# Kernel optimization log

Hardware: AMD Instinct MI355X
Metric: run time of the kernel (lower is better)

The kernel has to match this reference:

```python
import jax, jax.numpy as jnp
import numpy as np

N, E, IN, HID, OUT, B = 50000, 800000, 128, 128, 64, 4096
EPS = 1e-5


def setup_inputs() -> dict:
    key = jax.random.key(0)
    ks = jax.random.split(key, 12)
    x = jax.random.normal(ks[0], (N, IN), jnp.float32)
    edge_index = jax.random.randint(ks[1], (2, E), 0, N, dtype=jnp.int32).astype(jnp.int64)
    target_index = jax.random.randint(ks[2], (B,), 0, N, dtype=jnp.int32).astype(jnp.int64)

    def lin(k, i, o):
        return jax.random.normal(k, (i, o), jnp.float32) * (1.0 / np.sqrt(i))

    return {
        'x': x, 'edge_index': edge_index, 'target_index': target_index,
        'W0': lin(ks[3], IN, HID), 'b0': jnp.zeros((HID,), jnp.float32),
        'W1': lin(ks[4], HID, HID), 'b1': jnp.zeros((HID,), jnp.float32),
        'W2': lin(ks[5], HID, HID), 'b2': jnp.zeros((HID,), jnp.float32),
        'g0': jnp.ones((HID,), jnp.float32), 'bt0': jnp.zeros((HID,), jnp.float32),
        'g1': jnp.ones((HID,), jnp.float32), 'bt1': jnp.zeros((HID,), jnp.float32),
        'f1w': lin(ks[6], HID, HID), 'f1b': jnp.zeros((HID,), jnp.float32),
        'f2w': lin(ks[7], HID, OUT), 'f2b': jnp.zeros((OUT,), jnp.float32),
    }


def _gcn_layer(h, W, b, src, dst, norm):
    # GCNConv: D^-1/2 (A+I) D^-1/2 (h W) + b  (self-loops already in src/dst)
    h = h @ W                                        # [N, out]
    msg = h[src] * norm[:, None]                     # [E+N, out]
    return jax.ops.segment_sum(msg, dst, num_segments=N) + b


def _batchnorm(h, g, bt):
    mu = jnp.mean(h, axis=0)
    var = jnp.mean((h - mu) ** 2, axis=0)            # biased, as torch BN
    return g * (h - mu) * jax.lax.rsqrt(var + EPS) + bt


def reference(x, edge_index, target_index, W0, b0, W1, b1, W2, b2,
              g0, bt0, g1, bt1, f1w, f1b, f2w, f2b):
    loop = jnp.arange(N, dtype=edge_index.dtype)
    src = jnp.concatenate([edge_index[0], loop])
    dst = jnp.concatenate([edge_index[1], loop])
    deg = jax.ops.segment_sum(jnp.ones_like(dst, jnp.float32), dst, num_segments=N)
    dinv = jax.lax.rsqrt(deg)                        # deg >= 1 via self-loops
    norm = dinv[src] * dinv[dst]                     # [E+N]

    h = _gcn_layer(x, W0, b0, src, dst, norm)
    h = jax.nn.relu(_batchnorm(h, g0, bt0))
    h = _gcn_layer(h, W1, b1, src, dst, norm)
    h = jax.nn.relu(_batchnorm(h, g1, bt1))
    h = _gcn_layer(h, W2, b2, src, dst, norm)

    # target_index.unsqueeze(1).expand(-1,-1) -> [B,1]; pool squeezes dim 1
    t = h[target_index]                              # [B, HID]
    t = jax.nn.relu(t @ f1w + f1b)                   # FeedForwardNetwork layer1 (dropout=0)
    return t @ f2w + f2b                             # [B, OUT]
```

## Files before the change

### kernel.cpp

```cpp
#include <hip/hip_runtime.h>


static const int GNN5566_NN  = 50000;
static const int GNN5566_NE  = 800000;
static const int GNN5566_NB  = 4096;
static const int GNN5566_CAP = 64;

static const int GNN5566_NBUCK  = (GNN5566_NN + 63) / 64;
static const int GNN5566_NCHUNK = 128;
static const int GNN5566_CHUNK  = GNN5566_NE / GNN5566_NCHUNK;

static const int GNN5566_WSLOT = 17408;

typedef short gnn5566_s16x8 __attribute__((ext_vector_type(8)));
typedef float gnn5566_f32x4 __attribute__((ext_vector_type(4)));

static __device__ inline float gnn5566_b2f(unsigned short h){
  return __uint_as_float(((unsigned int)h) << 16);
}
static __device__ inline unsigned short gnn5566_f2b(float f){
  unsigned int u = __float_as_uint(f);
  u += 0x7fffu + ((u >> 16) & 1u);
  return (unsigned short)(u >> 16);
}
static __device__ inline float gnn5566_loadf(const void* p, long long i, int isF32){
  if (isF32) return ((const float*)p)[i];
  return gnn5566_b2f(((const unsigned short*)p)[i]);
}

__global__ void GNNEncoder_5566277616090_detect(const int* ei, const int* tgt,
                                                const void* W0, int* flags,
                                                float* stats){
  int t = threadIdx.x;
  if (t < 512) stats[t] = 0.0f;
  if (t < 64) {
    int o1 = ei[2*t + 1];
    int o2 = tgt[2*t + 1];
    unsigned int w = ((const unsigned int*)W0)[t];
    unsigned int e = (w >> 7) & 255u;
    int bf16ish = (e >= 96u && e <= 134u) ? 1 : 0;
    unsigned long long m1 = __ballot(o1 != 0);
    unsigned long long m2 = __ballot(o2 != 0);
    unsigned long long m3 = __ballot(bf16ish);
    if (t == 0) {
      flags[0] = (m1 == 0ull) ? 1 : 0;
      flags[1] = (m2 == 0ull) ? 1 : 0;
      flags[2] = (__popcll(m3) >= 56) ? 0 : 1;
    }
  }
}

__global__ void GNNEncoder_5566277616090_wprep(const void* W0, const void* W1,
                                               const void* W2, const void* f1w,
                                               const void* f2w, unsigned short* wT,
                                               const int* flags){
  __shared__ unsigned short lt[128][129];
  int b = blockIdx.x, tid = threadIdx.x;
  const void* src = (b == 0) ? W0 : (b == 1) ? W1 : (b == 2) ? W2
                  : (b == 3) ? f1w : f2w;
  int wide = (b != 4);
  int f32 = flags[2];
  int tot = wide ? 16384 : 8192;
  for (int i = tid; i < tot; i += 256) {
    int k = wide ? (i >> 7) : (i >> 6);
    int c = wide ? (i & 127) : (i & 63);
    lt[k][c] = f32 ? gnn5566_f2b(((const float*)src)[i])
                   : ((const unsigned short*)src)[i];
  }
  __syncthreads();
  unsigned short* out = wT + b * GNN5566_WSLOT;
  int wtot = wide ? 2048 : 1024;
  for (int j = tid; j < wtot; j += 256) {
    int c = j >> 4, k8 = (j & 15) << 3;
    unsigned int p0 = (unsigned int)lt[k8    ][c] | ((unsigned int)lt[k8 + 1][c] << 16);
    unsigned int p1 = (unsigned int)lt[k8 + 2][c] | ((unsigned int)lt[k8 + 3][c] << 16);
    unsigned int p2 = (unsigned int)lt[k8 + 4][c] | ((unsigned int)lt[k8 + 5][c] << 16);
    unsigned int p3 = (unsigned int)lt[k8 + 6][c] | ((unsigned int)lt[k8 + 7][c] << 16);
    uint4 v; v.x = p0; v.y = p1; v.z = p2; v.w = p3;
    *(uint4*)(out + c * 136 + k8) = v;
  }
}

__global__ void GNNEncoder_5566277616090_fillH(const int* ei, unsigned int* histT,
                                               const int* flags){
  __shared__ int h[GNN5566_NBUCK];
  int tid = threadIdx.x, chunk = blockIdx.x;
  for (int b = tid; b < GNN5566_NBUCK; b += 256) h[b] = 0;
  __syncthreads();
  int f = flags[0];
  int base = chunk * GNN5566_CHUNK;
  for (int i = tid; i < GNN5566_CHUNK; i += 256) {
    int e = base + i;
    int d = f ? ei[2*(GNN5566_NE + e)] : ei[GNN5566_NE + e];
    atomicAdd(&h[d >> 6], 1);
  }
  __syncthreads();
  for (int b = tid; b < GNN5566_NBUCK; b += 256)
    histT[b * GNN5566_NCHUNK + chunk] = (unsigned int)h[b];
}

__global__ void GNNEncoder_5566277616090_fillS1(unsigned int* histT, int* btot){
  int wv   = (int)(blockIdx.x * 4u + (threadIdx.x >> 6));
  int lane = threadIdx.x & 63;
  if (wv >= GNN5566_NBUCK) return;
  unsigned int* row = histT + wv * GNN5566_NCHUNK;
  uint2 v = ((const uint2*)row)[lane];
  int a = (int)v.x, b = (int)v.y;
  int s = a + b;
  int incl = s;
  #pragma unroll
  for (int off = 1; off < 64; off <<= 1) {
    int t = __shfl_up(incl, off, 64);
    if (lane >= off) incl += t;
  }
  int excl = incl - s;
  uint2 o; o.x = (unsigned int)excl; o.y = (unsigned int)(excl + a);
  ((uint2*)row)[lane] = o;
  if (lane == 63) btot[wv] = incl;
}

__global__ void GNNEncoder_5566277616090_fillS2(const int* btot, int* segStart){
  __shared__ int a[1024];
  int tid = threadIdx.x;
  int own = (tid < GNN5566_NBUCK) ? btot[tid] : 0;
  a[tid] = own;
  __syncthreads();
  for (int off = 1; off < 1024; off <<= 1) {
    int v = (tid >= off) ? a[tid - off] : 0;
    __syncthreads();
    a[tid] += v;
    __syncthreads();
  }
  if (tid < GNN5566_NBUCK) segStart[tid] = a[tid] - own;
  if (tid == 0) segStart[GNN5566_NBUCK] = GNN5566_NE;
}

__global__ void GNNEncoder_5566277616090_fillScatter(const int* ei,
                                                     const unsigned int* histT,
                                                     const int* segStart,
                                                     unsigned int* sorted,
                                                     const int* flags){
  __shared__ int cur[GNN5566_NBUCK];
  int tid = threadIdx.x, chunk = blockIdx.x;
  for (int b = tid; b < GNN5566_NBUCK; b += 256)
    cur[b] = (int)histT[b * GNN5566_NCHUNK + chunk] + segStart[b];
  __syncthreads();
  int f = flags[0];
  int base = chunk * GNN5566_CHUNK;
  for (int i = tid; i < GNN5566_CHUNK; i += 256) {
    int e = base + i;
    int s = f ? ei[2*e]                : ei[e];
    int d = f ? ei[2*(GNN5566_NE + e)] : ei[GNN5566_NE + e];
    int p = atomicAdd(&cur[d >> 6], 1);
    sorted[p] = ((unsigned int)s << 6) | (unsigned int)(d & 63);
  }
}

__global__ void GNNEncoder_5566277616090_fillB(const int* segStart,
                                               const unsigned int* sorted,
                                               unsigned short* colIdx16, int* cnt,
                                               float* dinv){
  __shared__ unsigned int lbuf[64 * 32];
  __shared__ int lcnt[64];
  int b   = blockIdx.x;
  int tid = threadIdx.x;
  if (tid < 64) lcnt[tid] = 0;
  __syncthreads();

  int s0 = segStart[b];
  int n  = segStart[b + 1] - s0;
  const unsigned int* bp = sorted + s0;
  unsigned short* lists = (unsigned short*)lbuf;
  for (int i = tid; i < n; i += 256) {
    unsigned int w = bp[i];
    int d = (int)(w & 63u);
    int s = (int)(w >> 6);
    int p = atomicAdd(&lcnt[d], 1);
    if (p < GNN5566_CAP) lists[d * 64 + p] = (unsigned short)s;
  }
  __syncthreads();

  if (tid < 64) {
    int node = b * 64 + tid;
    if (node < GNN5566_NN) {
      int c = lcnt[tid];
      cnt[node]  = c;
      dinv[node] = rsqrtf((float)(c + 1));
    }
  }
  unsigned int* out = (unsigned int*)colIdx16;
  for (int idx = tid; idx < 2048; idx += 256) {
    int d = idx >> 5;
    int node = b * 64 + d;
    if (node < GNN5566_NN)
      out[(long long)node * 32 + (idx & 31)] = lbuf[idx];
  }
}

__global__ void GNNEncoder_5566277616090_kernel(const void* A,
                                                const unsigned short* wT,
                                                unsigned short* Out, int nRows,
                                                const float* bnA, const float* bnC,
                                                const float* rowScale,
                                                const int* gather, const int* gatherFlag,
                                                const void* bias, int reluOut,
                                                int aExternal, const int* flags)
{
  __shared__ __align__(16) unsigned short gnnLw[128 * 136];
  int tid = threadIdx.x;
  int wF32 = flags[2];
  int aF32 = aExternal ? wF32 : 0;

  {
    const uint4* src = (const uint4*)wT;
    uint4* dst = (uint4*)gnnLw;
    for (int i = tid; i < 2176; i += 256) dst[i] = src[i];
  }
  __syncthreads();

  int wave = tid >> 6, lane = tid & 63;
  int q = lane >> 4, ln = lane & 15;
  int rowBase = blockIdx.x * 64 + wave * 16;
  int r  = rowBase + ln;
  int cr = (r < nRows) ? r : (nRows - 1);
  int ar = cr;
  if (gather) ar = (*gatherFlag) ? gather[2 * cr] : gather[cr];
  float rs = rowScale ? rowScale[cr] : 1.0f;

  gnn5566_s16x8 afr[4];
  #pragma unroll
  for (int kk = 0; kk < 4; ++kk) {
    int kb = kk * 32 + q * 8;
    float vals[8];
    if (aF32) {
      const float4* ap = (const float4*)A + (long long)ar * 32 + (kb >> 2);
      float4 u = ap[0], w = ap[1];
      vals[0] = u.x; vals[1] = u.y; vals[2] = u.z; vals[3] = u.w;
      vals[4] = w.x; vals[5] = w.y; vals[6] = w.z; vals[7] = w.w;
    } else {
      const uint4* ap = (const uint4*)A + (long long)ar * 16 + (kb >> 3);
      uint4 u = ap[0];
      vals[0] = gnn5566_b2f((unsigned short)(u.x & 0xffffu));
      vals[1] = gnn5566_b2f((unsigned short)(u.x >> 16));
      vals[2] = gnn5566_b2f((unsigned short)(u.y & 0xffffu));
      vals[3] = gnn5566_b2f((unsigned short)(u.y >> 16));
      vals[4] = gnn5566_b2f((unsigned short)(u.z & 0xffffu));
      vals[5] = gnn5566_b2f((unsigned short)(u.z >> 16));
      vals[6] = gnn5566_b2f((unsigned short)(u.w & 0xffffu));
      vals[7] = gnn5566_b2f((unsigned short)(u.w >> 16));
    }
    #pragma unroll
    for (int j = 0; j < 8; ++j) {
      float v = vals[j];
      if (bnA) { int k = kb + j; v = fmaxf(v * bnA[k] + bnC[k], 0.0f); }
      afr[kk][j] = (short)gnn5566_f2b(v * rs);
    }
  }

  gnn5566_f32x4 zero4;
  zero4[0] = 0.0f; zero4[1] = 0.0f; zero4[2] = 0.0f; zero4[3] = 0.0f;
  gnn5566_f32x4 acc[8];
  #pragma unroll
  for (int t = 0; t < 8; ++t) acc[t] = zero4;

  #pragma unroll
  for (int kk = 0; kk < 4; ++kk) {
    int kb = kk * 32 + q * 8;
    #pragma unroll
    for (int t = 0; t < 8; ++t) {
      gnn5566_s16x8 bfr = *(const gnn5566_s16x8*)(&gnnLw[(t * 16 + ln) * 136 + kb]);
      acc[t] = __builtin_amdgcn_mfma_f32_16x16x32_bf16(afr[kk], bfr, acc[t], 0, 0, 0);
    }
  }

  #pragma unroll
  for (int t = 0; t < 8; ++t) {
    int col = t * 16 + ln;
    float badd = bias ? gnn5566_loadf(bias, col, wF32) : 0.0f;
    #pragma unroll
    for (int rg = 0; rg < 4; ++rg) {
      int grow = rowBase + q * 4 + rg;
      if (grow < nRows) {
        float v = acc[t][rg] + badd;
        if (reluOut) v = fmaxf(v, 0.0f);
        Out[(long long)grow * 128 + col] = gnn5566_f2b(v);
      }
    }
  }
}

__global__ void GNNEncoder_5566277616090_g64(const unsigned short* A,
                                             const unsigned short* wT,
                                             void* Out, int nRows,
                                             const void* bias, const int* flags)
{
  __shared__ __align__(16) unsigned short gnnLw[64 * 136];
  int tid = threadIdx.x;
  int f32 = flags[2];

  {
    const uint4* src = (const uint4*)wT;
    uint4* dst = (uint4*)gnnLw;
    for (int i = tid; i < 1088; i += 256) dst[i] = src[i];
  }
  __syncthreads();

  int wave = tid >> 6, lane = tid & 63;
  int q = lane >> 4, ln = lane & 15;
  int rowBase = blockIdx.x * 64 + wave * 16;
  int r  = rowBase + ln;
  int cr = (r < nRows) ? r : (nRows - 1);

  gnn5566_s16x8 afr[4];
  #pragma unroll
  for (int kk = 0; kk < 4; ++kk) {
    int kb = kk * 32 + q * 8;
    const uint4* ap = (const uint4*)A + (long long)cr * 16 + (kb >> 3);
    uint4 u = ap[0];
    unsigned short e[8];
    e[0] = (unsigned short)(u.x & 0xffffu); e[1] = (unsigned short)(u.x >> 16);
    e[2] = (unsigned short)(u.y & 0xffffu); e[3] = (unsigned short)(u.y >> 16);
    e[4] = (unsigned short)(u.z & 0xffffu); e[5] = (unsigned short)(u.z >> 16);
    e[6] = (unsigned short)(u.w & 0xffffu); e[7] = (unsigned short)(u.w >> 16);
    #pragma unroll
    for (int j = 0; j < 8; ++j) afr[kk][j] = (short)e[j];
  }

  gnn5566_f32x4 zero4;
  zero4[0] = 0.0f; zero4[1] = 0.0f; zero4[2] = 0.0f; zero4[3] = 0.0f;
  gnn5566_f32x4 acc[4];
  #pragma unroll
  for (int t = 0; t < 4; ++t) acc[t] = zero4;

  #pragma unroll
  for (int kk = 0; kk < 4; ++kk) {
    int kb = kk * 32 + q * 8;
    #pragma unroll
    for (int t = 0; t < 4; ++t) {
      gnn5566_s16x8 bfr = *(const gnn5566_s16x8*)(&gnnLw[(t * 16 + ln) * 136 + kb]);
      acc[t] = __builtin_amdgcn_mfma_f32_16x16x32_bf16(afr[kk], bfr, acc[t], 0, 0, 0);
    }
  }

  #pragma unroll
  for (int t = 0; t < 4; ++t) {
    int col = t * 16 + ln;
    float badd = gnn5566_loadf(bias, col, f32);
    #pragma unroll
    for (int rg = 0; rg < 4; ++rg) {
      int grow = rowBase + q * 4 + rg;
      if (grow < nRows) {
        float v = acc[t][rg] + badd;
        if (f32) ((float*)Out)[(long long)grow * 64 + col] = v;
        else     ((unsigned short*)Out)[(long long)grow * 64 + col] = gnn5566_f2b(v);
      }
    }
  }
}

__global__ void GNNEncoder_5566277616090_agg(const unsigned short* hs,
                                             const unsigned short* colIdx16,
                                             const int* cnt, const float* dinv,
                                             const void* bias, unsigned short* ha,
                                             const int* flags)
{
  int gw = (int)((blockIdx.x * 256u + threadIdx.x) >> 6);
  if (gw >= GNN5566_NN) return;
  int lane = threadIdx.x & 63;
  const unsigned int* hrow = (const unsigned int*)hs;
  unsigned int sv = hrow[(long long)gw * 64 + lane];
  float a0 = __uint_as_float(sv << 16);
  float a1 = __uint_as_float(sv & 0xffff0000u);
  int m = cnt[gw]; if (m > GNN5566_CAP) m = GNN5566_CAP;
  const unsigned short* cp = colIdx16 + (long long)gw * GNN5566_CAP;
  const uint4* cp4 = (const uint4*)cp;
  int i = 0;
  for (; i + 8 <= m; i += 8) {
    uint4 iw = cp4[i >> 3];
    unsigned int s0 = iw.x & 0xffffu, s1 = iw.x >> 16;
    unsigned int s2 = iw.y & 0xffffu, s3 = iw.y >> 16;
    unsigned int s4 = iw.z & 0xffffu, s5 = iw.z >> 16;
    unsigned int s6 = iw.w & 0xffffu, s7 = iw.w >> 16;
    unsigned int v0 = hrow[(long long)s0 * 64 + lane];
    unsigned int v1 = hrow[(long long)s1 * 64 + lane];
    unsigned int v2 = hrow[(long long)s2 * 64 + lane];
    unsigned int v3 = hrow[(long long)s3 * 64 + lane];
    unsigned int v4 = hrow[(long long)s4 * 64 + lane];
    unsigned int v5 = hrow[(long long)s5 * 64 + lane];
    unsigned int v6 = hrow[(long long)s6 * 64 + lane];
    unsigned int v7 = hrow[(long long)s7 * 64 + lane];
    a0 += __uint_as_float(v0 << 16) + __uint_as_float(v1 << 16)
        + __uint_as_float(v2 << 16) + __uint_as_float(v3 << 16)
        + __uint_as_float(v4 << 16) + __uint_as_float(v5 << 16)
        + __uint_as_float(v6 << 16) + __uint_as_float(v7 << 16);
    a1 += __uint_as_float(v0 & 0xffff0000u) + __uint_as_float(v1 & 0xffff0000u)
        + __uint_as_float(v2 & 0xffff0000u) + __uint_as_float(v3 & 0xffff0000u)
        + __uint_as_float(v4 & 0xffff0000u) + __uint_as_float(v5 & 0xffff0000u)
        + __uint_as_float(v6 & 0xffff0000u) + __uint_as_float(v7 & 0xffff0000u);
  }
  for (; i < m; ++i) {
    unsigned int v = hrow[(long long)cp[i] * 64 + lane];
    a0 += __uint_as_float(v << 16);
    a1 += __uint_as_float(v & 0xffff0000u);
  }
  float s = dinv[gw];
  int f32 = flags[2];
  float o0 = a0 * s + gnn5566_loadf(bias, lane * 2,     f32);
  float o1 = a1 * s + gnn5566_loadf(bias, lane * 2 + 1, f32);
  unsigned int packed = (unsigned int)gnn5566_f2b(o0)
                      | (((unsigned int)gnn5566_f2b(o1)) << 16);
  ((unsigned int*)ha)[(long long)gw * 64 + lane] = packed;
}

__global__ void GNNEncoder_5566277616090_stats(const unsigned short* ha, float* stats){
  __shared__ float red[256];
  const unsigned int* h32 = (const unsigned int*)ha;
  int tid = threadIdx.x;
  int cp2 = tid & 63, sub = tid >> 6;
  float s0 = 0.0f, s1 = 0.0f, q0 = 0.0f, q1 = 0.0f;
  for (int r = blockIdx.x * 4 + sub; r < GNN5566_NN; r += 1024) {
    unsigned int v = h32[(long long)r * 64 + cp2];
    float a = __uint_as_float(v << 16);
    float b = __uint_as_float(v & 0xffff0000u);
    s0 += a; q0 += a * a; s1 += b; q1 += b * b;
  }
  red[tid] = s0; __syncthreads();
  if (sub == 0) atomicAdd(&stats[2*cp2],
      red[cp2] + red[64+cp2] + red[128+cp2] + red[192+cp2]);
  __syncthreads();
  red[tid] = s1; __syncthreads();
  if (sub == 0) atomicAdd(&stats[2*cp2 + 1],
      red[cp2] + red[64+cp2] + red[128+cp2] + red[192+cp2]);
  __syncthreads();
  red[tid] = q0; __syncthreads();
  if (sub == 0) atomicAdd(&stats[128 + 2*cp2],
      red[cp2] + red[64+cp2] + red[128+cp2] + red[192+cp2]);
  __syncthreads();
  red[tid] = q1; __syncthreads();
  if (sub == 0) atomicAdd(&stats[128 + 2*cp2 + 1],
      red[cp2] + red[64+cp2] + red[128+cp2] + red[192+cp2]);
}

__global__ void GNNEncoder_5566277616090_bnfin(const float* stats, const void* g,
                                               const void* bt, float* bnA, float* bnC,
                                               const int* flags){
  int c = threadIdx.x;
  if (c >= 128) return;
  int f32 = flags[2];
  float invN = 1.0f / (float)GNN5566_NN;
  float mu  = stats[c] * invN;
  float var = stats[128 + c] * invN - mu * mu;
  if (var < 0.0f) var = 0.0f;
  float a = gnn5566_loadf(g, c, f32) * rsqrtf(var + 1e-5f);
  bnA[c] = a;
  bnC[c] = gnn5566_loadf(bt, c, f32) - mu * a;
}

extern "C" void kernel_launch(void* const* d_in, const int* in_sizes, int n_in,
                              void* d_out, int out_size, void* d_ws, size_t ws_size,
                              hipStream_t stream)
{
  const void* x   = d_in[0];
  const int*  ei  = (const int*)d_in[1];
  const int*  tgt = (const int*)d_in[2];
  const void* W0  = d_in[3];
  const void* b0  = d_in[4];
  const void* W1  = d_in[5];
  const void* b1  = d_in[6];
  const void* W2  = d_in[7];
  const void* b2  = d_in[8];
  const void* g0  = d_in[9];
  const void* bt0 = d_in[10];
  const void* g1  = d_in[11];
  const void* bt1 = d_in[12];
  const void* f1w = d_in[13];
  const void* f1b = d_in[14];
  const void* f2w = d_in[15];
  const void* fb2 = d_in[16];

  char* ws = (char*)d_ws;
  int*            segStart = (int*)           (ws + 0);
  int*            btot     = (int*)           (ws + 4096);
  int*            cnt      = (int*)           (ws + 8192);
  float*          dinv     = (float*)         (ws + 208896);
  unsigned short* wT       = (unsigned short*)(ws + 409600);
  unsigned int*   histT    = (unsigned int*)  (ws + 586752);
  unsigned int*   sorted   = (unsigned int*)  (ws + 987648);
  unsigned short* colIdx16 = (unsigned short*)(ws + 4188160);
  unsigned short* hs       = (unsigned short*)(ws + 10588160);
  unsigned short* ha       = (unsigned short*)(ws + 23388160);
  unsigned short* ub       = (unsigned short*)(ws + 36188160);
  float*          stats    = (float*)         (ws + 37236992);
  float*          bn       = (float*)         (ws + 37239040);
  int*            flags    = (int*)           (ws + 37241088);

  float* bn0A = bn;       float* bn0C = bn + 128;
  float* bn1A = bn + 256; float* bn1C = bn + 384;

  GNNEncoder_5566277616090_detect<<<1, 512, 0, stream>>>(ei, tgt, W0, flags, stats);
  GNNEncoder_5566277616090_wprep <<<5, 256, 0, stream>>>(W0, W1, W2, f1w, f2w, wT, flags);
  GNNEncoder_5566277616090_fillH <<<GNN5566_NCHUNK, 256, 0, stream>>>(ei, histT, flags);
  GNNEncoder_5566277616090_fillS1<<<196, 256, 0, stream>>>(histT, btot);
  GNNEncoder_5566277616090_fillS2<<<1, 1024, 0, stream>>>(btot, segStart);
  GNNEncoder_5566277616090_fillScatter<<<GNN5566_NCHUNK, 256, 0, stream>>>(
      ei, histT, segStart, sorted, flags);
  GNNEncoder_5566277616090_fillB <<<GNN5566_NBUCK, 256, 0, stream>>>(
      segStart, sorted, colIdx16, cnt, dinv);

  const int gemmGrid = (GNN5566_NN + 63) / 64;

  GNNEncoder_5566277616090_kernel<<<gemmGrid, 256, 0, stream>>>(
      x, wT, hs, GNN5566_NN, (const float*)0, (const float*)0, dinv,
      (const int*)0, (const int*)0, (const void*)0, 0, 1, flags);
  GNNEncoder_5566277616090_agg  <<<12500, 256, 0, stream>>>(hs, colIdx16, cnt, dinv, b0, ha, flags);
  GNNEncoder_5566277616090_stats<<<256, 256, 0, stream>>>(ha, stats);
  GNNEncoder_5566277616090_bnfin<<<1, 128, 0, stream>>>(stats, g0, bt0, bn0A, bn0C, flags);

  GNNEncoder_5566277616090_kernel<<<gemmGrid, 256, 0, stream>>>(
      ha, wT + GNN5566_WSLOT, hs, GNN5566_NN, bn0A, bn0C, dinv,
      (const int*)0, (const int*)0, (const void*)0, 0, 0, flags);
  GNNEncoder_5566277616090_agg  <<<12500, 256, 0, stream>>>(hs, colIdx16, cnt, dinv, b1, ha, flags);
  GNNEncoder_5566277616090_stats<<<256, 256, 0, stream>>>(ha, stats + 256);
  GNNEncoder_5566277616090_bnfin<<<1, 128, 0, stream>>>(stats + 256, g1, bt1, bn1A, bn1C, flags);

  GNNEncoder_5566277616090_kernel<<<gemmGrid, 256, 0, stream>>>(
      ha, wT + 2 * GNN5566_WSLOT, hs, GNN5566_NN, bn1A, bn1C, dinv,
      (const int*)0, (const int*)0, (const void*)0, 0, 0, flags);
  GNNEncoder_5566277616090_agg  <<<12500, 256, 0, stream>>>(hs, colIdx16, cnt, dinv, b2, ha, flags);

  GNNEncoder_5566277616090_kernel<<<64, 256, 0, stream>>>(
      ha, wT + 3 * GNN5566_WSLOT, ub, GNN5566_NB,
      (const float*)0, (const float*)0, (const float*)0,
      tgt, flags + 1, f1b, 1, 0, flags);
  GNNEncoder_5566277616090_g64<<<64, 256, 0, stream>>>(
      ub, wT + 4 * GNN5566_WSLOT, d_out, GNN5566_NB, fb2, flags);
}
```

Measured before the change: 387.1 us.

## Fuse small kernels, stage GEMM epilogue through LDS, fuse FFN layers

Several small launches are merged: flag detection moves into the weight-prep kernel, BN finalisation runs in the last block of the stats kernel via an atomic done counter, and the two FFN GEMMs become one kernel with the hidden tile kept in LDS. The main GEMM caches BN scale/shift and bias in shared memory and writes its output tile through LDS for coalesced 16-byte stores. The histogram chunk count doubles and the int64 index reads use int2 loads. The aim is to cut launch overhead and uncoalesced stores, at the cost of more LDS use and a last-block synchronisation pattern.

```diff
diff --git a/kernel.cpp b/kernel.cpp
--- a/kernel.cpp
+++ b/kernel.cpp
@@ -7,7 +7,7 @@
 static const int GNN5566_CAP = 64;
 
 static const int GNN5566_NBUCK  = (GNN5566_NN + 63) / 64;
-static const int GNN5566_NCHUNK = 128;
+static const int GNN5566_NCHUNK = 256;
 static const int GNN5566_CHUNK  = GNN5566_NE / GNN5566_NCHUNK;
 
 static const int GNN5566_WSLOT = 17408;
@@ -28,38 +28,47 @@
   return gnn5566_b2f(((const unsigned short*)p)[i]);
 }
 
-__global__ void GNNEncoder_5566277616090_detect(const int* ei, const int* tgt,
-                                                const void* W0, int* flags,
-                                                float* stats){
-  int t = threadIdx.x;
-  if (t < 512) stats[t] = 0.0f;
-  if (t < 64) {
-    int o1 = ei[2*t + 1];
-    int o2 = tgt[2*t + 1];
-    unsigned int w = ((const unsigned int*)W0)[t];
-    unsigned int e = (w >> 7) & 255u;
-    int bf16ish = (e >= 96u && e <= 134u) ? 1 : 0;
-    unsigned long long m1 = __ballot(o1 != 0);
-    unsigned long long m2 = __ballot(o2 != 0);
-    unsigned long long m3 = __ballot(bf16ish);
-    if (t == 0) {
-      flags[0] = (m1 == 0ull) ? 1 : 0;
-      flags[1] = (m2 == 0ull) ? 1 : 0;
-      flags[2] = (__popcll(m3) >= 56) ? 0 : 1;
-    }
-  }
-}
-
 __global__ void GNNEncoder_5566277616090_wprep(const void* W0, const void* W1,
                                                const void* W2, const void* f1w,
                                                const void* f2w, unsigned short* wT,
-                                               const int* flags){
+                                               const int* ei, const int* tgt,
+                                               int* flags, float* stats, int* done){
   __shared__ unsigned short lt[128][129];
+  __shared__ int sF32;
   int b = blockIdx.x, tid = threadIdx.x;
+
+  if (b == 5) {
+    for (int i = tid; i < 512; i += 256) stats[i] = 0.0f;
+    if (tid < 2) done[tid] = 0;
+    if (tid < 64) {
+      int o1 = ei[2*tid + 1];
+      int o2 = tgt[2*tid + 1];
+      unsigned int w = ((const unsigned int*)W0)[tid];
+      unsigned int e = (w >> 7) & 255u;
+      unsigned long long m1 = __ballot(o1 != 0);
+      unsigned long long m2 = __ballot(o2 != 0);
+      unsigned long long m3 = __ballot(e >= 96u && e <= 134u);
+      if (tid == 0) {
+        flags[0] = (m1 == 0ull) ? 1 : 0;
+        flags[1] = (m2 == 0ull) ? 1 : 0;
+        flags[2] = (__popcll(m3) >= 56) ? 0 : 1;
+      }
+    }
+    return;
+  }
+
+  if (tid < 64) {
+    unsigned int w = ((const unsigned int*)W0)[tid];
+    unsigned int e = (w >> 7) & 255u;
+    unsigned long long m3 = __ballot(e >= 96u && e <= 134u);
+    if (tid == 0) sF32 = (__popcll(m3) >= 56) ? 0 : 1;
+  }
+  __syncthreads();
+  int f32 = sF32;
+
   const void* src = (b == 0) ? W0 : (b == 1) ? W1 : (b == 2) ? W2
                   : (b == 3) ? f1w : f2w;
   int wide = (b != 4);
-  int f32 = flags[2];
   int tot = wide ? 16384 : 8192;
   for (int i = tid; i < tot; i += 256) {
     int k = wide ? (i >> 7) : (i >> 6);
@@ -91,7 +100,7 @@
   int base = chunk * GNN5566_CHUNK;
   for (int i = tid; i < GNN5566_CHUNK; i += 256) {
     int e = base + i;
-    int d = f ? ei[2*(GNN5566_NE + e)] : ei[GNN5566_NE + e];
+    int d = f ? ((const int2*)ei)[GNN5566_NE + e].x : ei[GNN5566_NE + e];
     atomicAdd(&h[d >> 6], 1);
   }
   __syncthreads();
@@ -104,9 +113,9 @@
   int lane = threadIdx.x & 63;
   if (wv >= GNN5566_NBUCK) return;
   unsigned int* row = histT + wv * GNN5566_NCHUNK;
-  uint2 v = ((const uint2*)row)[lane];
-  int a = (int)v.x, b = (int)v.y;
-  int s = a + b;
+  uint4 v = ((const uint4*)row)[lane];
+  int a = (int)v.x, b = (int)v.y, c = (int)v.z, d = (int)v.w;
+  int s = a + b + c + d;
   int incl = s;
   #pragma unroll
   for (int off = 1; off < 64; off <<= 1) {
@@ -114,8 +123,12 @@
     if (lane >= off) incl += t;
   }
   int excl = incl - s;
-  uint2 o; o.x = (unsigned int)excl; o.y = (unsigned int)(excl + a);
-  ((uint2*)row)[lane] = o;
+  uint4 o;
+  o.x = (unsigned int)excl;
+  o.y = (unsigned int)(excl + a);
+  o.z = (unsigned int)(excl + a + b);
+  o.w = (unsigned int)(excl + a + b + c);
+  ((uint4*)row)[lane] = o;
   if (lane == 63) btot[wv] = incl;
 }
 
@@ -149,8 +162,8 @@
   int base = chunk * GNN5566_CHUNK;
   for (int i = tid; i < GNN5566_CHUNK; i += 256) {
     int e = base + i;
-    int s = f ? ei[2*e]                : ei[e];
-    int d = f ? ei[2*(GNN5566_NE + e)] : ei[GNN5566_NE + e];
+    int s = f ? ((const int2*)ei)[e].x                : ei[e];
+    int d = f ? ((const int2*)ei)[GNN5566_NE + e].x   : ei[GNN5566_NE + e];
     int p = atomicAdd(&cur[d >> 6], 1);
     sorted[p] = ((unsigned int)s << 6) | (unsigned int)(d & 63);
   }
@@ -202,11 +215,11 @@
                                                 unsigned short* Out, int nRows,
                                                 const float* bnA, const float* bnC,
                                                 const float* rowScale,
-                                                const int* gather, const int* gatherFlag,
                                                 const void* bias, int reluOut,
                                                 int aExternal, const int* flags)
 {
   __shared__ __align__(16) unsigned short gnnLw[128 * 136];
+  __shared__ float lbnA[128], lbnC[128], lbias[128];
   int tid = threadIdx.x;
   int wF32 = flags[2];
   int aF32 = aExternal ? wF32 : 0;
@@ -215,6 +228,11 @@
     const uint4* src = (const uint4*)wT;
     uint4* dst = (uint4*)gnnLw;
     for (int i = tid; i < 2176; i += 256) dst[i] = src[i];
+  }
+  if (tid < 128) {
+    lbnA[tid]  = bnA  ? bnA[tid] : 0.0f;
+    lbnC[tid]  = bnC  ? bnC[tid] : 0.0f;
+    lbias[tid] = bias ? gnn5566_loadf(bias, tid, wF32) : 0.0f;
   }
   __syncthreads();
 
@@ -223,9 +241,8 @@
   int rowBase = blockIdx.x * 64 + wave * 16;
   int r  = rowBase + ln;
   int cr = (r < nRows) ? r : (nRows - 1);
-  int ar = cr;
-  if (gather) ar = (*gatherFlag) ? gather[2 * cr] : gather[cr];
   float rs = rowScale ? rowScale[cr] : 1.0f;
+  int useBN = (bnA != 0);
 
   gnn5566_s16x8 afr[4];
   #pragma unroll
@@ -233,12 +250,12 @@
     int kb = kk * 32 + q * 8;
     float vals[8];
     if (aF32) {
-      const float4* ap = (const float4*)A + (long long)ar * 32 + (kb >> 2);
+      const float4* ap = (const float4*)A + (long long)cr * 32 + (kb >> 2);
       float4 u = ap[0], w = ap[1];
       vals[0] = u.x; vals[1] = u.y; vals[2] = u.z; vals[3] = u.w;
       vals[4] = w.x; vals[5] = w.y; vals[6] = w.z; vals[7] = w.w;
     } else {
-      const uint4* ap = (const uint4*)A + (long long)ar * 16 + (kb >> 3);
+      const uint4* ap = (const uint4*)A + (long long)cr * 16 + (kb >> 3);
       uint4 u = ap[0];
       vals[0] = gnn5566_b2f((unsigned short)(u.x & 0xffffu));
       vals[1] = gnn5566_b2f((unsigned short)(u.x >> 16));
@@ -249,12 +266,20 @@
       vals[6] = gnn5566_b2f((unsigned short)(u.w & 0xffffu));
       vals[7] = gnn5566_b2f((unsigned short)(u.w >> 16));
     }
-    #pragma unroll
-    for (int j = 0; j < 8; ++j) {
-      float v = vals[j];
-      if (bnA) { int k = kb + j; v = fmaxf(v * bnA[k] + bnC[k], 0.0f); }
-      afr[kk][j] = (short)gnn5566_f2b(v * rs);
-    }
+    if (useBN) {
+      float4 a0 = *(const float4*)&lbnA[kb], a1 = *(const float4*)&lbnA[kb + 4];
+      float4 c0 = *(const float4*)&lbnC[kb], c1 = *(const float4*)&lbnC[kb + 4];
+      vals[0] = fmaxf(vals[0] * a0.x + c0.x, 0.0f);
+      vals[1] = fmaxf(vals[1] * a0.y + c0.y, 0.0f);
+      vals[2] = fmaxf(vals[2] * a0.z + c0.z, 0.0f);
+      vals[3] = fmaxf(vals[3] * a0.w + c0.w, 0.0f);
+      vals[4] = fmaxf(vals[4] * a1.x + c1.x, 0.0f);
+      vals[5] = fmaxf(vals[5] * a1.y + c1.y, 0.0f);
+      vals[6] = fmaxf(vals[6] * a1.z + c1.z, 0.0f);
+      vals[7] = fmaxf(vals[7] * a1.w + c1.w, 0.0f);
+    }
+    #pragma unroll
+    for (int j = 0; j < 8; ++j) afr[kk][j] = (short)gnn5566_f2b(vals[j] * rs);
   }
 
   gnn5566_f32x4 zero4;
@@ -273,49 +298,70 @@
     }
   }
 
+  __syncthreads();
   #pragma unroll
   for (int t = 0; t < 8; ++t) {
     int col = t * 16 + ln;
-    float badd = bias ? gnn5566_loadf(bias, col, wF32) : 0.0f;
+    float badd = lbias[col];
     #pragma unroll
     for (int rg = 0; rg < 4; ++rg) {
-      int grow = rowBase + q * 4 + rg;
-      if (grow < nRows) {
-        float v = acc[t][rg] + badd;
-        if (reluOut) v = fmaxf(v, 0.0f);
-        Out[(long long)grow * 128 + col] = gnn5566_f2b(v);
-      }
-    }
-  }
-}
-
-__global__ void GNNEncoder_5566277616090_g64(const unsigned short* A,
-                                             const unsigned short* wT,
-                                             void* Out, int nRows,
-                                             const void* bias, const int* flags)
+      float v = acc[t][rg] + badd;
+      if (reluOut) v = fmaxf(v, 0.0f);
+      gnnLw[(wave * 16 + q * 4 + rg) * 136 + col] = gnn5566_f2b(v);
+    }
+  }
+  __syncthreads();
+  int tRowBase = blockIdx.x * 64;
+  for (int j = tid; j < 1024; j += 256) {
+    int rr = j >> 4, c4 = j & 15;
+    int grow = tRowBase + rr;
+    if (grow < nRows) {
+      uint4 v = *(const uint4*)&gnnLw[rr * 136 + c4 * 8];
+      *(uint4*)&Out[(long long)grow * 128 + c4 * 8] = v;
+    }
+  }
+}
+
+__global__ void GNNEncoder_5566277616090_ffn(const unsigned short* A,
+                                             const unsigned short* wT3,
+                                             const unsigned short* wT4,
+                                             void* Out, const int* tgt,
+                                             const int* tgtFlag,
+                                             const void* f1b, const void* fb2,
+                                             const int* flags)
 {
-  __shared__ __align__(16) unsigned short gnnLw[64 * 136];
+  __shared__ __align__(16) unsigned short lwA[128 * 136];
+  __shared__ __align__(16) unsigned short lwB[64 * 136];
+  __shared__ __align__(16) unsigned short ep[64 * 136];
+  __shared__ float lb1[128];
+  __shared__ float lb2[64];
   int tid = threadIdx.x;
   int f32 = flags[2];
 
   {
-    const uint4* src = (const uint4*)wT;
-    uint4* dst = (uint4*)gnnLw;
-    for (int i = tid; i < 1088; i += 256) dst[i] = src[i];
-  }
+    const uint4* sA = (const uint4*)wT3;
+    uint4* dA = (uint4*)lwA;
+    for (int i = tid; i < 2176; i += 256) dA[i] = sA[i];
+    const uint4* sB = (const uint4*)wT4;
+    uint4* dB = (uint4*)lwB;
+    for (int i = tid; i < 1088; i += 256) dB[i] = sB[i];
+  }
+  if (tid < 128) lb1[tid] = gnn5566_loadf(f1b, tid, f32);
+  if (tid < 64)  lb2[tid] = gnn5566_loadf(fb2, tid, f32);
   __syncthreads();
 
   int wave = tid >> 6, lane = tid & 63;
   int q = lane >> 4, ln = lane & 15;
   int rowBase = blockIdx.x * 64 + wave * 16;
   int r  = rowBase + ln;
-  int cr = (r < nRows) ? r : (nRows - 1);
+  int cr = (r < GNN5566_NB) ? r : (GNN5566_NB - 1);
+  int ar = (*tgtFlag) ? tgt[2 * cr] : tgt[cr];
 
   gnn5566_s16x8 afr[4];
   #pragma unroll
   for (int kk = 0; kk < 4; ++kk) {
     int kb = kk * 32 + q * 8;
-    const uint4* ap = (const uint4*)A + (long long)cr * 16 + (kb >> 3);
+    const uint4* ap = (const uint4*)A + (long long)ar * 16 + (kb >> 3);
     uint4 u = ap[0];
     unsigned short e[8];
     e[0] = (unsigned short)(u.x & 0xffffu); e[1] = (unsigned short)(u.x >> 16);
@@ -328,29 +374,57 @@
 
   gnn5566_f32x4 zero4;
   zero4[0] = 0.0f; zero4[1] = 0.0f; zero4[2] = 0.0f; zero4[3] = 0.0f;
-  gnn5566_f32x4 acc[4];
-  #pragma unroll
-  for (int t = 0; t < 4; ++t) acc[t] = zero4;
-
+  gnn5566_f32x4 acc[8];
+  #pragma unroll
+  for (int t = 0; t < 8; ++t) acc[t] = zero4;
   #pragma unroll
   for (int kk = 0; kk < 4; ++kk) {
     int kb = kk * 32 + q * 8;
     #pragma unroll
+    for (int t = 0; t < 8; ++t) {
+      gnn5566_s16x8 bfr = *(const gnn5566_s16x8*)(&lwA[(t * 16 + ln) * 136 + kb]);
+      acc[t] = __builtin_amdgcn_mfma_f32_16x16x32_bf16(afr[kk], bfr, acc[t], 0, 0, 0);
+    }
+  }
+  #pragma unroll
+  for (int t = 0; t < 8; ++t) {
+    int col = t * 16 + ln;
+    float badd = lb1[col];
+    #pragma unroll
+    for (int rg = 0; rg < 4; ++rg) {
+      float v = fmaxf(acc[t][rg] + badd, 0.0f);
+      ep[(wave * 16 + q * 4 + rg) * 136 + col] = gnn5566_f2b(v);
+    }
+  }
+  __syncthreads();
+
+  gnn5566_s16x8 afr2[4];
+  #pragma unroll
+  for (int kk = 0; kk < 4; ++kk) {
+    int kb = kk * 32 + q * 8;
+    afr2[kk] = *(const gnn5566_s16x8*)(&ep[(wave * 16 + ln) * 136 + kb]);
+  }
+  gnn5566_f32x4 acc2[4];
+  #pragma unroll
+  for (int t = 0; t < 4; ++t) acc2[t] = zero4;
+  #pragma unroll
+  for (int kk = 0; kk < 4; ++kk) {
+    int kb = kk * 32 + q * 8;
+    #pragma unroll
     for (int t = 0; t < 4; ++t) {
-      gnn5566_s16x8 bfr = *(const gnn5566_s16x8*)(&gnnLw[(t * 16 + ln) * 136 + kb]);
-      acc[t] = __builtin_amdgcn_mfma_f32_16x16x32_bf16(afr[kk], bfr, acc[t], 0, 0, 0);
-    }
-  }
-
+      gnn5566_s16x8 bfr = *(const gnn5566_s16x8*)(&lwB[(t * 16 + ln) * 136 + kb]);
+      acc2[t] = __builtin_amdgcn_mfma_f32_16x16x32_bf16(afr2[kk], bfr, acc2[t], 0, 0, 0);
+    }
+  }
   #pragma unroll
   for (int t = 0; t < 4; ++t) {
     int col = t * 16 + ln;
-    float badd = gnn5566_loadf(bias, col, f32);
+    float badd = lb2[col];
     #pragma unroll
     for (int rg = 0; rg < 4; ++rg) {
       int grow = rowBase + q * 4 + rg;
-      if (grow < nRows) {
-        float v = acc[t][rg] + badd;
+      if (grow < GNN5566_NB) {
+        float v = acc2[t][rg] + badd;
         if (f32) ((float*)Out)[(long long)grow * 64 + col] = v;
         else     ((unsigned short*)Out)[(long long)grow * 64 + col] = gnn5566_f2b(v);
       }
@@ -412,8 +486,12 @@
   ((unsigned int*)ha)[(long long)gw * 64 + lane] = packed;
 }
 
-__global__ void GNNEncoder_5566277616090_stats(const unsigned short* ha, float* stats){
+__global__ void GNNEncoder_5566277616090_stats(const unsigned short* ha, float* statsL,
+                                               const void* g, const void* bt,
+                                               float* bnA, float* bnC,
+                                               const int* flags, int* doneCtr){
   __shared__ float red[256];
+  __shared__ int lastFlag;
   const unsigned int* h32 = (const unsigned int*)ha;
   int tid = threadIdx.x;
   int cp2 = tid & 63, sub = tid >> 6;
@@ -425,35 +503,37 @@
     s0 += a; q0 += a * a; s1 += b; q1 += b * b;
   }
   red[tid] = s0; __syncthreads();
-  if (sub == 0) atomicAdd(&stats[2*cp2],
+  if (sub == 0) atomicAdd(&statsL[2*cp2],
       red[cp2] + red[64+cp2] + red[128+cp2] + red[192+cp2]);
   __syncthreads();
   red[tid] = s1; __syncthreads();
-  if (sub == 0) atomicAdd(&stats[2*cp2 + 1],
+  if (sub == 0) atomicAdd(&statsL[2*cp2 + 1],
       red[cp2] + red[64+cp2] + red[128+cp2] + red[192+cp2]);
   __syncthreads();
   red[tid] = q0; __syncthreads();
-  if (sub == 0) atomicAdd(&stats[128 + 2*cp2],
+  if (sub == 0) atomicAdd(&statsL[128 + 2*cp2],
       red[cp2] + red[64+cp2] + red[128+cp2] + red[192+cp2]);
   __syncthreads();
   red[tid] = q1; __syncthreads();
-  if (sub == 0) atomicAdd(&stats[128 + 2*cp2 + 1],
+  if (sub == 0) atomicAdd(&statsL[128 + 2*cp2 + 1],
       red[cp2] + red[64+cp2] + red[128+cp2] + red[192+cp2]);
-}
-
-__global__ void GNNEncoder_5566277616090_bnfin(const float* stats, const void* g,
-                                               const void* bt, float* bnA, float* bnC,
-                                               const int* flags){
-  int c = threadIdx.x;
-  if (c >= 128) return;
-  int f32 = flags[2];
-  float invN = 1.0f / (float)GNN5566_NN;
-  float mu  = stats[c] * invN;
-  float var = stats[128 + c] * invN - mu * mu;
-  if (var < 0.0f) var = 0.0f;
-  float a = gnn5566_loadf(g, c, f32) * rsqrtf(var + 1e-5f);
-  bnA[c] = a;
-  bnC[c] = gnn5566_loadf(bt, c, f32) - mu * a;
+  __syncthreads();
+
+  __threadfence();
+  if (tid == 0) lastFlag = (atomicAdd(doneCtr, 1) == (int)gridDim.x - 1);
+  __syncthreads();
+  if (lastFlag && tid < 128) {
+    int f32 = flags[2];
+    float sum = atomicAdd(&statsL[tid], 0.0f);
+    float sq  = atomicAdd(&statsL[128 + tid], 0.0f);
+    float invN = 1.0f / (float)GNN5566_NN;
+    float mu  = sum * invN;
+    float var = sq * invN - mu * mu;
+    if (var < 0.0f) var = 0.0f;
+    float a = gnn5566_loadf(g, tid, f32) * rsqrtf(var + 1e-5f);
+    bnA[tid] = a;
+    bnC[tid] = gnn5566_loadf(bt, tid, f32) - mu * a;
+  }
 }
 
 extern "C" void kernel_launch(void* const* d_in, const int* in_sizes, int n_in,
@@ -484,21 +564,21 @@
   int*            cnt      = (int*)           (ws + 8192);
   float*          dinv     = (float*)         (ws + 208896);
   unsigned short* wT       = (unsigned short*)(ws + 409600);
-  unsigned int*   histT    = (unsigned int*)  (ws + 586752);
-  unsigned int*   sorted   = (unsigned int*)  (ws + 987648);
-  unsigned short* colIdx16 = (unsigned short*)(ws + 4188160);
-  unsigned short* hs       = (unsigned short*)(ws + 10588160);
-  unsigned short* ha       = (unsigned short*)(ws + 23388160);
-  unsigned short* ub       = (unsigned short*)(ws + 36188160);
-  float*          stats    = (float*)         (ws + 37236992);
-  float*          bn       = (float*)         (ws + 37239040);
-  int*            flags    = (int*)           (ws + 37241088);
+  unsigned int*   histT    = (unsigned int*)  (ws + 583936);
+  unsigned int*   sorted   = (unsigned int*)  (ws + 1384960);
+  unsigned short* colIdx16 = (unsigned short*)(ws + 4585216);
+  unsigned short* hs       = (unsigned short*)(ws + 10985472);
+  unsigned short* ha       = (unsigned short*)(ws + 23785728);
+  float*          stats    = (float*)         (ws + 36585984);
+  float*          bn       = (float*)         (ws + 36588032);
+  int*            flags    = (int*)           (ws + 36590080);
+  int*            done     = (int*)           (ws + 36590336);
 
   float* bn0A = bn;       float* bn0C = bn + 128;
   float* bn1A = bn + 256; float* bn1C = bn + 384;
 
-  GNNEncoder_5566277616090_detect<<<1, 512, 0, stream>>>(ei, tgt, W0, flags, stats);
-  GNNEncoder_5566277616090_wprep <<<5, 256, 0, stream>>>(W0, W1, W2, f1w, f2w, wT, flags);
+  GNNEncoder_5566277616090_wprep <<<6, 256, 0, stream>>>(
+      W0, W1, W2, f1w, f2w, wT, ei, tgt, flags, stats, done);
   GNNEncoder_5566277616090_fillH <<<GNN5566_NCHUNK, 256, 0, stream>>>(ei, histT, flags);
   GNNEncoder_5566277616090_fillS1<<<196, 256, 0, stream>>>(histT, btot);
   GNNEncoder_5566277616090_fillS2<<<1, 1024, 0, stream>>>(btot, segStart);
@@ -511,27 +591,24 @@
 
   GNNEncoder_5566277616090_kernel<<<gemmGrid, 256, 0, stream>>>(
       x, wT, hs, GNN5566_NN, (const float*)0, (const float*)0, dinv,
-      (const int*)0, (const int*)0, (const void*)0, 0, 1, flags);
+      (const void*)0, 0, 1, flags);
   GNNEncoder_5566277616090_agg  <<<12500, 256, 0, stream>>>(hs, colIdx16, cnt, dinv, b0, ha, flags);
-  GNNEncoder_5566277616090_stats<<<256, 256, 0, stream>>>(ha, stats);
-  GNNEncoder_5566277616090_bnfin<<<1, 128, 0, stream>>>(stats, g0, bt0, bn0A, bn0C, flags);
+  GNNEncoder_5566277616090_stats<<<256, 256, 0, stream>>>(
+      ha, stats, g0, bt0, bn0A, bn0C, flags, done);
 
   GNNEncoder_5566277616090_kernel<<<gemmGrid, 256, 0, stream>>>(
       ha, wT + GNN5566_WSLOT, hs, GNN5566_NN, bn0A, bn0C, dinv,
-      (const int*)0, (const int*)0, (const void*)0, 0, 0, flags);
+      (const void*)0, 0, 0, flags);
   GNNEncoder_5566277616090_agg  <<<12500, 256, 0, stream>>>(hs, colIdx16, cnt, dinv, b1, ha, flags);
-  GNNEncoder_5566277616090_stats<<<256, 256, 0, stream>>>(ha, stats + 256);
-  GNNEncoder_5566277616090_bnfin<<<1, 128, 0, stream>>>(stats + 256, g1, bt1, bn1A, bn1C, flags);
+  GNNEncoder_5566277616090_stats<<<256, 256, 0, stream>>>(
+      ha, stats + 256, g1, bt1, bn1A, bn1C, flags, done + 1);
 
   GNNEncoder_5566277616090_kernel<<<gemmGrid, 256, 0, stream>>>(
       ha, wT + 2 * GNN5566_WSLOT, hs, GNN5566_NN, bn1A, bn1C, dinv,
-      (const int*)0, (const int*)0, (const void*)0, 0, 0, flags);
+      (const void*)0, 0, 0, flags);
   GNNEncoder_5566277616090_agg  <<<12500, 256, 0, stream>>>(hs, colIdx16, cnt, dinv, b2, ha, flags);
 
-  GNNEncoder_5566277616090_kernel<<<64, 256, 0, stream>>>(
-      ha, wT + 3 * GNN5566_WSLOT, ub, GNN5566_NB,
-      (const float*)0, (const float*)0, (const float*)0,
-      tgt, flags + 1, f1b, 1, 0, flags);
-  GNNEncoder_5566277616090_g64<<<64, 256, 0, stream>>>(
-      ub, wT + 4 * GNN5566_WSLOT, d_out, GNN5566_NB, fb2, flags);
-}
+  GNNEncoder_5566277616090_ffn<<<64, 256, 0, stream>>>(
+      ha, wT + 3 * GNN5566_WSLOT, wT + 4 * GNN5566_WSLOT, d_out,
+      tgt, flags + 1, f1b, fb2, flags);
+}
```

Measured after the change: 374.9 us. -3.1%, faster.
